# Kernel optimization log

Measured on AMD Instinct MI355X. Metric: run time of the kernel, lower is better.

Reference implementation:

```python
import jax, jax.numpy as jnp
import numpy as np

B, S, K, N = 4, 2048, 4096, 4096   # batch, seq, infeatures, outfeatures
GROUP = 128                        # quantization group size along K
N_OUT = 128                        # outlier features (last columns of x)


def setup_inputs() -> dict:
    key = jax.random.key(0)
    ks = jax.random.split(key, 6)
    x = jax.random.normal(ks[0], (B, S, K), dtype=jnp.float32)
    # unpacked 4-bit integer weights in [0, 16)
    qweight = jax.random.randint(ks[1], (N, K), 0, 16, dtype=jnp.int32)
    # per-group scales and scaled zeros: [numgroup, N] = [K//GROUP, N]
    scales = jax.random.uniform(ks[2], (K // GROUP, N), dtype=jnp.float32, minval=0.005, maxval=0.02)
    # scaled_zeros = -zeros * scales in the original pack(); keep them negative-ish
    scaled_zeros = -jax.random.uniform(ks[3], (K // GROUP, N), dtype=jnp.float32, minval=0.0, maxval=0.16)
    oweight = jax.random.normal(ks[4], (N, N_OUT), dtype=jnp.float32) * 0.02
    bias = jax.random.normal(ks[5], (N,), dtype=jnp.float32) * 0.02
    return {"x": x, "qweight": qweight, "scales": scales,
            "scaled_zeros": scaled_zeros, "oweight": oweight, "bias": bias}


def reference(x, qweight, scales, scaled_zeros, oweight, bias):
    # gemm_4bit: dequantize W[n,k] = q[n,k]*scales[k//G, n] + scaled_zeros[k//G, n]
    g = x.shape[-1] // scales.shape[0]
    scales_full = jnp.repeat(scales, g, axis=0).T        # [N, K]
    zeros_full = jnp.repeat(scaled_zeros, g, axis=0).T   # [N, K]
    W = qweight.astype(scales.dtype) * scales_full + zeros_full  # [N, K]
    y = jnp.einsum('bsk,nk->bsn', x, W)
    # fused outlier fp16 linear on the last N_OUT input features + bias
    n_out = oweight.shape[1]
    y = y + jnp.einsum('bso,no->bsn', x[..., -n_out:], oweight) + bias
    return y
```

## Files before the change

### kernel.cpp

```cpp
#include <hip/hip_runtime.h>

#define K_ 4096
#define N_ 4096
#define M_ 8192
#define NOUT_ 128
#define NT_ (K_ / 64)

typedef __bf16 bf16x8 __attribute__((ext_vector_type(8)));
typedef float f32x4 __attribute__((ext_vector_type(4)));
typedef unsigned short ushort8 __attribute__((ext_vector_type(8)));

__device__ __forceinline__ unsigned short f2bf(float f) {
  unsigned u = __builtin_bit_cast(unsigned, f);
  u += 0x7fffu + ((u >> 16) & 1u);
  return (unsigned short)(u >> 16);
}

__global__ void cvt_x_kernel(const float4* __restrict__ x4, ushort8* __restrict__ xb) {
  const int t = blockIdx.x * 256 + threadIdx.x;
  float4 a = x4[2 * t];
  float4 b = x4[2 * t + 1];
  ushort8 o;
  o[0] = f2bf(a.x); o[1] = f2bf(a.y); o[2] = f2bf(a.z); o[3] = f2bf(a.w);
  o[4] = f2bf(b.x); o[5] = f2bf(b.y); o[6] = f2bf(b.z); o[7] = f2bf(b.w);
  xb[t] = o;
}

__global__ void dequant_kernel(const int4* __restrict__ q4,
                               const float* __restrict__ scales,
                               const float* __restrict__ zeros,
                               const float* __restrict__ ow,
                               ushort8* __restrict__ wb) {
  const int t = blockIdx.x * 256 + threadIdx.x;
  const int n = t >> 9;
  const int k = (t & 511) << 3;
  const int g = k >> 7;
  const float s = scales[g * N_ + n];
  const float z = zeros[g * N_ + n];
  int4 qa = q4[2 * t], qb = q4[2 * t + 1];
  float f[8];
  f[0] = qa.x * s + z; f[1] = qa.y * s + z; f[2] = qa.z * s + z; f[3] = qa.w * s + z;
  f[4] = qb.x * s + z; f[5] = qb.y * s + z; f[6] = qb.z * s + z; f[7] = qb.w * s + z;
  if (k >= K_ - NOUT_) {
    const float4* o4 = (const float4*)(ow + n * NOUT_ + (k - (K_ - NOUT_)));
    float4 oa = o4[0], ob = o4[1];
    f[0] += oa.x; f[1] += oa.y; f[2] += oa.z; f[3] += oa.w;
    f[4] += ob.x; f[5] += ob.y; f[6] += ob.z; f[7] += ob.w;
  }
  ushort8 r;
  #pragma unroll
  for (int i = 0; i < 8; ++i) r[i] = f2bf(f[i]);
  wb[t] = r;
}

#define AS1 __attribute__((address_space(1)))
#define AS3 __attribute__((address_space(3)))

#define STAGE_A(h, kt, ubase)                                                      \
  do {                                                                             \
    __builtin_amdgcn_global_load_lds(                                              \
        (AS1 void*)(sgA0 + (size_t)(h) * 128 * K_ + (kt) * 64),                    \
        (AS3 void*)((ubase) + w * 1024), 16, 0, 0);                                \
    __builtin_amdgcn_global_load_lds(                                              \
        (AS1 void*)(sgA1 + (size_t)(h) * 128 * K_ + (kt) * 64),                    \
        (AS3 void*)((ubase) + 8192 + w * 1024), 16, 0, 0);                         \
  } while (0)

#define STAGE_B(h, kt, ubase)                                                      \
  do {                                                                             \
    __builtin_amdgcn_global_load_lds(                                              \
        (AS1 void*)(sgB0 + (size_t)(h) * 128 * K_ + (kt) * 64),                    \
        (AS3 void*)((ubase) + w * 1024), 16, 0, 0);                                \
    __builtin_amdgcn_global_load_lds(                                              \
        (AS1 void*)(sgB1 + (size_t)(h) * 128 * K_ + (kt) * 64),                    \
        (AS3 void*)((ubase) + 8192 + w * 1024), 16, 0, 0);                         \
  } while (0)

__global__ __launch_bounds__(512, 2) void gemm_kernel(
    const unsigned short* __restrict__ xb,
    const unsigned short* __restrict__ wb,
    const float* __restrict__ bias,
    float* __restrict__ out) {
  __shared__ __attribute__((aligned(16))) char smem[131072];

  const int tid  = threadIdx.x;
  const int w    = tid >> 6;
  const int lane = tid & 63;
  const int q    = lane >> 4;
  const int l16  = lane & 15;
  const int wr   = w >> 2;
  const int wc   = w & 3;

  const int id  = blockIdx.y * 16 + blockIdx.x;
  const int id2 = (id & 7) * 64 + (id >> 3);
  const int m0  = (id2 >> 4) * 256;
  const int n0  = (id2 & 15) * 256;

  const int rr = w * 8 + (lane >> 3);
  const int cg = (lane & 7) ^ ((lane >> 3) & 7);
  const unsigned short* sgA0 = xb + (size_t)(m0 + rr) * K_ + cg * 8;
  const unsigned short* sgA1 = xb + (size_t)(m0 + 64 + rr) * K_ + cg * 8;
  const unsigned short* sgB0 = wb + (size_t)(n0 + rr) * K_ + cg * 8;
  const unsigned short* sgB1 = wb + (size_t)(n0 + 64 + rr) * K_ + cg * 8;

  const char* pA_base = smem + wr * 16384 + l16 * 128;
  const char* pB_base = smem + 65536 + (wc >> 1) * 16384 +
                        ((wc & 1) * 64 + l16) * 128;
  const int sl0 = ((0 + q) ^ (l16 & 7)) * 16;
  const int sl1 = ((4 + q) ^ (l16 & 7)) * 16;

  f32x4 acc[8][4] = {};

  STAGE_B(0, 0, smem + 65536);
  STAGE_B(1, 0, smem + 65536 + 16384);
  STAGE_A(0, 0, smem);
  STAGE_A(1, 0, smem + 16384);
  STAGE_B(0, 1, smem + 65536 + 32768);
  STAGE_B(1, 1, smem + 65536 + 32768 + 16384);
  STAGE_A(0, 1, smem + 32768);
  asm volatile("s_waitcnt vmcnt(6)" ::: "memory");
  __builtin_amdgcn_s_barrier();

  for (int t = 0; t < NT_; ++t) {
    const int curo = (t & 1) * 32768;
    const int nxto = ((t + 1) & 1) * 32768;
    const char* cA = pA_base + curo;
    const char* cB = pB_base + curo;

    bf16x8 a[4][2], b[4][2];

    #pragma unroll
    for (int f = 0; f < 4; ++f) {
      a[f][0] = *(const bf16x8*)(cA + f * 2048 + sl0);
      a[f][1] = *(const bf16x8*)(cA + f * 2048 + sl1);
    }
    #pragma unroll
    for (int j = 0; j < 4; ++j) {
      b[j][0] = *(const bf16x8*)(cB + j * 2048 + sl0);
      b[j][1] = *(const bf16x8*)(cB + j * 2048 + sl1);
    }
    if (t + 1 < NT_) STAGE_A(1, t + 1, smem + nxto + 16384);
    __builtin_amdgcn_s_barrier();
    asm volatile("s_waitcnt lgkmcnt(0)" ::: "memory");
    __builtin_amdgcn_sched_barrier(0);
    __builtin_amdgcn_s_setprio(1);
    #pragma unroll
    for (int f = 0; f < 4; ++f)
      #pragma unroll
      for (int j = 0; j < 2; ++j) {
        acc[f][j] = __builtin_amdgcn_mfma_f32_16x16x32_bf16(a[f][0], b[j][0], acc[f][j], 0, 0, 0);
        acc[f][j] = __builtin_amdgcn_mfma_f32_16x16x32_bf16(a[f][1], b[j][1], acc[f][j], 0, 0, 0);
      }
    __builtin_amdgcn_s_setprio(0);
    __builtin_amdgcn_s_barrier();

    if (t + 2 < NT_) STAGE_B(0, t + 2, smem + 65536 + curo);
    __builtin_amdgcn_s_setprio(1);
    #pragma unroll
    for (int f = 0; f < 4; ++f)
      #pragma unroll
      for (int j = 0; j < 2; ++j) {
        acc[f][2 + j] = __builtin_amdgcn_mfma_f32_16x16x32_bf16(a[f][0], b[2 + j][0], acc[f][2 + j], 0, 0, 0);
        acc[f][2 + j] = __builtin_amdgcn_mfma_f32_16x16x32_bf16(a[f][1], b[2 + j][1], acc[f][2 + j], 0, 0, 0);
      }
    __builtin_amdgcn_s_setprio(0);
    __builtin_amdgcn_s_barrier();

    #pragma unroll
    for (int f = 0; f < 4; ++f) {
      a[f][0] = *(const bf16x8*)(cA + 8192 + f * 2048 + sl0);
      a[f][1] = *(const bf16x8*)(cA + 8192 + f * 2048 + sl1);
    }
    if (t + 2 < NT_) STAGE_B(1, t + 2, smem + 65536 + curo + 16384);
    __builtin_amdgcn_s_barrier();
    asm volatile("s_waitcnt lgkmcnt(0)" ::: "memory");
    __builtin_amdgcn_sched_barrier(0);
    __builtin_amdgcn_s_setprio(1);
    #pragma unroll
    for (int f = 0; f < 4; ++f)
      #pragma unroll
      for (int j = 0; j < 2; ++j) {
        acc[4 + f][j] = __builtin_amdgcn_mfma_f32_16x16x32_bf16(a[f][0], b[j][0], acc[4 + f][j], 0, 0, 0);
        acc[4 + f][j] = __builtin_amdgcn_mfma_f32_16x16x32_bf16(a[f][1], b[j][1], acc[4 + f][j], 0, 0, 0);
      }
    __builtin_amdgcn_s_setprio(0);
    __builtin_amdgcn_s_barrier();

    if (t + 2 < NT_) STAGE_A(0, t + 2, smem + curo);
    __builtin_amdgcn_s_setprio(1);
    #pragma unroll
    for (int f = 0; f < 4; ++f)
      #pragma unroll
      for (int j = 0; j < 2; ++j) {
        acc[4 + f][2 + j] = __builtin_amdgcn_mfma_f32_16x16x32_bf16(a[f][0], b[2 + j][0], acc[4 + f][2 + j], 0, 0, 0);
        acc[4 + f][2 + j] = __builtin_amdgcn_mfma_f32_16x16x32_bf16(a[f][1], b[2 + j][1], acc[4 + f][2 + j], 0, 0, 0);
      }
    __builtin_amdgcn_s_setprio(0);
    if (t + 2 < NT_) {
      asm volatile("s_waitcnt vmcnt(6)" ::: "memory");
    } else {
      asm volatile("s_waitcnt vmcnt(0)" ::: "memory");
    }
    __builtin_amdgcn_s_barrier();
  }

  float bv[4];
  #pragma unroll
  for (int j = 0; j < 4; ++j)
    bv[j] = bias[n0 + wc * 64 + j * 16 + l16];

  #pragma unroll
  for (int i = 0; i < 8; ++i) {
    const int mrow = m0 + wr * 128 + i * 16 + q * 4;
    #pragma unroll
    for (int j = 0; j < 4; ++j) {
      const int n = n0 + wc * 64 + j * 16 + l16;
      float* op = out + (size_t)mrow * N_ + n;
      #pragma unroll
      for (int r = 0; r < 4; ++r)
        op[(size_t)r * N_] = acc[i][j][r] + bv[j];
    }
  }
}

extern "C" void kernel_launch(void* const* d_in, const int* in_sizes, int n_in,
                              void* d_out, int out_size, void* d_ws, size_t ws_size,
                              hipStream_t stream) {
  const float* x      = (const float*)d_in[0];
  const int*   qw     = (const int*)d_in[1];
  const float* scales = (const float*)d_in[2];
  const float* zeros  = (const float*)d_in[3];
  const float* ow     = (const float*)d_in[4];
  const float* bias   = (const float*)d_in[5];
  float* out = (float*)d_out;

  unsigned short* xb = (unsigned short*)d_ws;
  unsigned short* wb = xb + (size_t)M_ * K_;

  cvt_x_kernel<<<(M_ * K_ / 8) / 256, 256, 0, stream>>>((const float4*)x, (ushort8*)xb);
  dequant_kernel<<<(N_ * K_ / 8) / 256, 256, 0, stream>>>((const int4*)qw, scales, zeros, ow,
                                                          (ushort8*)wb);
  dim3 grid(N_ / 256, M_ / 256);
  gemm_kernel<<<grid, 512, 0, stream>>>(xb, wb, bias, out);
}
```

Before: 495.9 us.

## Prefetch LDS fragments into registers to overlap reads with MFMA phases

Restructures the GEMM main loop so A and B fragments for the next phase are read from LDS while MFMAs of the current phase run, instead of waiting on lgkmcnt(0) before each compute block. Global-to-LDS staging is regrouped to issue both halves of A or B together, the prologue now prefetches a full extra A tile, and the vmcnt thresholds change to match. sched_barriers pin the ordering. It aims to hide LDS latency, at the cost of more live registers and a tighter hazard ordering on shared buffers.

```diff
diff --git a/kernel.cpp b/kernel.cpp
--- a/kernel.cpp
+++ b/kernel.cpp
@@ -55,6 +55,7 @@
 
 #define AS1 __attribute__((address_space(1)))
 #define AS3 __attribute__((address_space(3)))
+#define SB() __builtin_amdgcn_sched_barrier(0)
 
 #define STAGE_A(h, kt, ubase)                                                      \
   do {                                                                             \
@@ -104,12 +105,14 @@
   const unsigned short* sgB1 = wb + (size_t)(n0 + 64 + rr) * K_ + cg * 8;
 
   const char* pA_base = smem + wr * 16384 + l16 * 128;
-  const char* pB_base = smem + 65536 + (wc >> 1) * 16384 +
-                        ((wc & 1) * 64 + l16) * 128;
+  const char* pB_base = smem + 65536 + (wc >> 1) * 16384 + ((wc & 1) * 64 + l16) * 128;
   const int sl0 = ((0 + q) ^ (l16 & 7)) * 16;
   const int sl1 = ((4 + q) ^ (l16 & 7)) * 16;
 
   f32x4 acc[8][4] = {};
+  bf16x8 aR[4][2];
+  bf16x8 b0R[2][2];
+  bf16x8 b1R[2][2];
 
   STAGE_B(0, 0, smem + 65536);
   STAGE_B(1, 0, smem + 65536 + 16384);
@@ -118,90 +121,107 @@
   STAGE_B(0, 1, smem + 65536 + 32768);
   STAGE_B(1, 1, smem + 65536 + 32768 + 16384);
   STAGE_A(0, 1, smem + 32768);
-  asm volatile("s_waitcnt vmcnt(6)" ::: "memory");
+  STAGE_A(1, 1, smem + 32768 + 16384);
+  asm volatile("s_waitcnt vmcnt(8)" ::: "memory");
   __builtin_amdgcn_s_barrier();
+  SB();
+  #pragma unroll
+  for (int f = 0; f < 4; ++f) {
+    aR[f][0] = *(const bf16x8*)(pA_base + f * 2048 + sl0);
+    aR[f][1] = *(const bf16x8*)(pA_base + f * 2048 + sl1);
+  }
+  #pragma unroll
+  for (int j = 0; j < 2; ++j) {
+    b0R[j][0] = *(const bf16x8*)(pB_base + j * 2048 + sl0);
+    b0R[j][1] = *(const bf16x8*)(pB_base + j * 2048 + sl1);
+  }
 
   for (int t = 0; t < NT_; ++t) {
     const int curo = (t & 1) * 32768;
     const int nxto = ((t + 1) & 1) * 32768;
-    const char* cA = pA_base + curo;
-    const char* cB = pB_base + curo;
-
-    bf16x8 a[4][2], b[4][2];
-
+    const char* cA  = pA_base + curo;
+    const char* cB  = pB_base + curo;
+    const char* cAn = pA_base + nxto;
+    const char* cBn = pB_base + nxto;
+
+    #pragma unroll
+    for (int j = 0; j < 2; ++j) {
+      b1R[j][0] = *(const bf16x8*)(cB + (2 + j) * 2048 + sl0);
+      b1R[j][1] = *(const bf16x8*)(cB + (2 + j) * 2048 + sl1);
+    }
+    __builtin_amdgcn_s_setprio(1);
+    #pragma unroll
+    for (int f = 0; f < 4; ++f)
+      #pragma unroll
+      for (int j = 0; j < 2; ++j) {
+        acc[f][j] = __builtin_amdgcn_mfma_f32_16x16x32_bf16(aR[f][0], b0R[j][0], acc[f][j], 0, 0, 0);
+        acc[f][j] = __builtin_amdgcn_mfma_f32_16x16x32_bf16(aR[f][1], b0R[j][1], acc[f][j], 0, 0, 0);
+      }
+    __builtin_amdgcn_s_setprio(0);
+    SB(); __builtin_amdgcn_s_barrier(); SB();
+
+    __builtin_amdgcn_s_setprio(1);
+    #pragma unroll
+    for (int f = 0; f < 4; ++f)
+      #pragma unroll
+      for (int j = 0; j < 2; ++j) {
+        acc[f][2 + j] = __builtin_amdgcn_mfma_f32_16x16x32_bf16(aR[f][0], b1R[j][0], acc[f][2 + j], 0, 0, 0);
+        acc[f][2 + j] = __builtin_amdgcn_mfma_f32_16x16x32_bf16(aR[f][1], b1R[j][1], acc[f][2 + j], 0, 0, 0);
+      }
+    __builtin_amdgcn_s_setprio(0);
     #pragma unroll
     for (int f = 0; f < 4; ++f) {
-      a[f][0] = *(const bf16x8*)(cA + f * 2048 + sl0);
-      a[f][1] = *(const bf16x8*)(cA + f * 2048 + sl1);
-    }
-    #pragma unroll
-    for (int j = 0; j < 4; ++j) {
-      b[j][0] = *(const bf16x8*)(cB + j * 2048 + sl0);
-      b[j][1] = *(const bf16x8*)(cB + j * 2048 + sl1);
-    }
-    if (t + 1 < NT_) STAGE_A(1, t + 1, smem + nxto + 16384);
-    __builtin_amdgcn_s_barrier();
-    asm volatile("s_waitcnt lgkmcnt(0)" ::: "memory");
-    __builtin_amdgcn_sched_barrier(0);
-    __builtin_amdgcn_s_setprio(1);
-    #pragma unroll
-    for (int f = 0; f < 4; ++f)
-      #pragma unroll
-      for (int j = 0; j < 2; ++j) {
-        acc[f][j] = __builtin_amdgcn_mfma_f32_16x16x32_bf16(a[f][0], b[j][0], acc[f][j], 0, 0, 0);
-        acc[f][j] = __builtin_amdgcn_mfma_f32_16x16x32_bf16(a[f][1], b[j][1], acc[f][j], 0, 0, 0);
-      }
-    __builtin_amdgcn_s_setprio(0);
-    __builtin_amdgcn_s_barrier();
-
-    if (t + 2 < NT_) STAGE_B(0, t + 2, smem + 65536 + curo);
-    __builtin_amdgcn_s_setprio(1);
-    #pragma unroll
-    for (int f = 0; f < 4; ++f)
-      #pragma unroll
-      for (int j = 0; j < 2; ++j) {
-        acc[f][2 + j] = __builtin_amdgcn_mfma_f32_16x16x32_bf16(a[f][0], b[2 + j][0], acc[f][2 + j], 0, 0, 0);
-        acc[f][2 + j] = __builtin_amdgcn_mfma_f32_16x16x32_bf16(a[f][1], b[2 + j][1], acc[f][2 + j], 0, 0, 0);
-      }
-    __builtin_amdgcn_s_setprio(0);
-    __builtin_amdgcn_s_barrier();
-
-    #pragma unroll
-    for (int f = 0; f < 4; ++f) {
-      a[f][0] = *(const bf16x8*)(cA + 8192 + f * 2048 + sl0);
-      a[f][1] = *(const bf16x8*)(cA + 8192 + f * 2048 + sl1);
-    }
-    if (t + 2 < NT_) STAGE_B(1, t + 2, smem + 65536 + curo + 16384);
-    __builtin_amdgcn_s_barrier();
-    asm volatile("s_waitcnt lgkmcnt(0)" ::: "memory");
-    __builtin_amdgcn_sched_barrier(0);
-    __builtin_amdgcn_s_setprio(1);
-    #pragma unroll
-    for (int f = 0; f < 4; ++f)
-      #pragma unroll
-      for (int j = 0; j < 2; ++j) {
-        acc[4 + f][j] = __builtin_amdgcn_mfma_f32_16x16x32_bf16(a[f][0], b[j][0], acc[4 + f][j], 0, 0, 0);
-        acc[4 + f][j] = __builtin_amdgcn_mfma_f32_16x16x32_bf16(a[f][1], b[j][1], acc[4 + f][j], 0, 0, 0);
-      }
-    __builtin_amdgcn_s_setprio(0);
-    __builtin_amdgcn_s_barrier();
-
-    if (t + 2 < NT_) STAGE_A(0, t + 2, smem + curo);
-    __builtin_amdgcn_s_setprio(1);
-    #pragma unroll
-    for (int f = 0; f < 4; ++f)
-      #pragma unroll
-      for (int j = 0; j < 2; ++j) {
-        acc[4 + f][2 + j] = __builtin_amdgcn_mfma_f32_16x16x32_bf16(a[f][0], b[2 + j][0], acc[4 + f][2 + j], 0, 0, 0);
-        acc[4 + f][2 + j] = __builtin_amdgcn_mfma_f32_16x16x32_bf16(a[f][1], b[2 + j][1], acc[4 + f][2 + j], 0, 0, 0);
-      }
-    __builtin_amdgcn_s_setprio(0);
+      aR[f][0] = *(const bf16x8*)(cA + 8192 + f * 2048 + sl0);
+      aR[f][1] = *(const bf16x8*)(cA + 8192 + f * 2048 + sl1);
+    }
+    SB(); __builtin_amdgcn_s_barrier(); SB();
+
     if (t + 2 < NT_) {
-      asm volatile("s_waitcnt vmcnt(6)" ::: "memory");
+      STAGE_B(0, t + 2, smem + 65536 + curo);
+      STAGE_B(1, t + 2, smem + 65536 + curo + 16384);
+    }
+    __builtin_amdgcn_s_setprio(1);
+    #pragma unroll
+    for (int f = 0; f < 4; ++f)
+      #pragma unroll
+      for (int j = 0; j < 2; ++j) {
+        acc[4 + f][2 + j] = __builtin_amdgcn_mfma_f32_16x16x32_bf16(aR[f][0], b1R[j][0], acc[4 + f][2 + j], 0, 0, 0);
+        acc[4 + f][2 + j] = __builtin_amdgcn_mfma_f32_16x16x32_bf16(aR[f][1], b1R[j][1], acc[4 + f][2 + j], 0, 0, 0);
+      }
+    __builtin_amdgcn_s_setprio(0);
+    if (t + 2 < NT_) {
+      asm volatile("s_waitcnt vmcnt(4)" ::: "memory");
     } else {
       asm volatile("s_waitcnt vmcnt(0)" ::: "memory");
     }
-    __builtin_amdgcn_s_barrier();
+    SB(); __builtin_amdgcn_s_barrier(); SB();
+
+    if (t + 2 < NT_) {
+      STAGE_A(0, t + 2, smem + curo);
+      STAGE_A(1, t + 2, smem + curo + 16384);
+    }
+    __builtin_amdgcn_s_setprio(1);
+    #pragma unroll
+    for (int f = 0; f < 4; ++f)
+      #pragma unroll
+      for (int j = 0; j < 2; ++j) {
+        acc[4 + f][j] = __builtin_amdgcn_mfma_f32_16x16x32_bf16(aR[f][0], b0R[j][0], acc[4 + f][j], 0, 0, 0);
+        acc[4 + f][j] = __builtin_amdgcn_mfma_f32_16x16x32_bf16(aR[f][1], b0R[j][1], acc[4 + f][j], 0, 0, 0);
+      }
+    __builtin_amdgcn_s_setprio(0);
+    if (t + 1 < NT_) {
+      #pragma unroll
+      for (int f = 0; f < 4; ++f) {
+        aR[f][0] = *(const bf16x8*)(cAn + f * 2048 + sl0);
+        aR[f][1] = *(const bf16x8*)(cAn + f * 2048 + sl1);
+      }
+      #pragma unroll
+      for (int j = 0; j < 2; ++j) {
+        b0R[j][0] = *(const bf16x8*)(cBn + j * 2048 + sl0);
+        b0R[j][1] = *(const bf16x8*)(cBn + j * 2048 + sl1);
+      }
+    }
+    SB(); __builtin_amdgcn_s_barrier(); SB();
   }
 
   float bv[4];
```

Result: no change. 494.8 us (-0.2%).
